# Kernel optimization log

Hardware: AMD Instinct MI355X
Metric: run time of the kernel (lower is better)

Reference implementation:

```python
import jax, jax.numpy as jnp
import numpy as np

DIM = 4096
N_HEADS = 32
N_KV = 8
HD = 128
SW = 4096          # sliding window / cache length
B = 32             # max_batch_size (decode batch)
MAX_SEQ = 8192
START_POS = 4000
CURRENT_POS = 4000

def _nearest_32(n):
    return ((n + 31) // 32) * 32

PADDED_LEN = min(_nearest_32(START_POS + 1), SW)  # 4032

def _rope_tables():
    inv_freq = 1.0 / (10000.0 ** (np.arange(0, HD, 2, dtype=np.float32) / HD))
    t = np.arange(MAX_SEQ, dtype=np.float32)
    freqs = np.outer(t, inv_freq)                       # [MAX_SEQ, HD/2]
    emb = np.concatenate([freqs, freqs], axis=-1)       # [MAX_SEQ, HD]
    return jnp.asarray(np.cos(emb)), jnp.asarray(np.sin(emb))

def rotate_half(u):
    u1, u2 = jnp.split(u, 2, axis=-1)
    return jnp.concatenate([-u2, u1], axis=-1)

def setup_inputs() -> dict:
    key = jax.random.key(0)
    ks = jax.random.split(key, 6)
    cos_cached, sin_cached = _rope_tables()
    return {
        "x": jax.random.normal(ks[0], (1, 1, B, DIM), jnp.float32),
        "wqkv": jax.random.normal(ks[1], (DIM, DIM + 2 * N_KV * HD), jnp.float32) * 0.02,
        "wo": jax.random.normal(ks[2], (DIM, DIM), jnp.float32) * 0.02,
        "cache_k": jax.random.normal(ks[3], (B, N_KV, SW, HD), jnp.float32) * 0.5,
        "cache_v": jax.random.normal(ks[4], (B, N_KV, SW, HD), jnp.float32) * 0.5,
        "cos_cached": cos_cached,
        "sin_cached": sin_cached,
        "attn_mask": jnp.zeros((B, N_HEADS, 1, PADDED_LEN), jnp.float32),
        "start_pos": START_POS,
        "current_pos": CURRENT_POS,
    }

def reference(x, wqkv, wo, cache_k, cache_v, cos_cached, sin_cached, attn_mask,
              start_pos, current_pos):
    group = N_HEADS // N_KV
    padded_len = min(_nearest_32(start_pos + 1), SW)
    scale = 1.0 / jnp.sqrt(jnp.float32(HD))

    # fused QKV projection: x (1,1,B,DIM) @ wqkv -> (B, DIM + 2*N_KV*HD)
    xqkv = x[0, 0] @ wqkv
    q = xqkv[:, :DIM].reshape(B, N_HEADS, HD)
    k = xqkv[:, DIM:DIM + N_KV * HD].reshape(B, N_KV, HD)
    v = xqkv[:, DIM + N_KV * HD:].reshape(B, N_KV, HD)

    # rotary embedding at position start_pos (single decode token)
    cos = cos_cached[start_pos]   # [HD]
    sin = sin_cached[start_pos]
    q = q * cos + rotate_half(q) * sin
    k = k * cos + rotate_half(k) * sin

    # sliding-window KV cache update at current_pos
    cache_k = cache_k.at[:, :, current_pos, :].set(k)
    cache_v = cache_v.at[:, :, current_pos, :].set(v)
    keys = cache_k[:, :, :padded_len, :]     # [B, N_KV, L, HD]
    values = cache_v[:, :, :padded_len, :]

    # grouped attention: q heads grouped by kv head
    qg = q.reshape(B, N_KV, group, HD)
    scores = jnp.einsum('bkgd,bkld->bkgl', qg, keys) * scale
    scores = scores + attn_mask.reshape(B, N_KV, group, padded_len)
    probs = jax.nn.softmax(scores, axis=-1)
    out = jnp.einsum('bkgl,bkld->bkgd', probs, values)   # [B, N_KV, group, HD]

    # concat heads and output projection
    dense = out.reshape(B, DIM) @ wo
    return dense.reshape(1, 1, B, DIM)
```

## Files before the change

kernel.cpp:

```cpp
#include <hip/hip_runtime.h>
#include <hip/hip_bf16.h>

typedef unsigned int u32;
typedef unsigned short u16;

__device__ __forceinline__ u16 f2bf(float f){ u32 x; __builtin_memcpy(&x,&f,4); u32 r=(x+0x7fffu+((x>>16)&1u))>>16; return (u16)r; }
__device__ __forceinline__ float lo2f(u32 u){ u32 x=u<<16; float f; __builtin_memcpy(&f,&x,4); return f; }
__device__ __forceinline__ float hi2f(u32 u){ u32 x=u&0xffff0000u; float f; __builtin_memcpy(&f,&x,4); return f; }

__global__ __launch_bounds__(256) void transpose_x(
    const float* __restrict__ x, float* __restrict__ xt)
{
    __shared__ float ld[32][65];
    const int t = threadIdx.x;
    const int g = blockIdx.x;
    #pragma unroll
    for (int i=0;i<8;++i) {
        const int e = i*256 + t;
        const int b = e >> 6, dd = e & 63;
        ld[b][dd] = x[(size_t)b*4096 + g*64 + dd];
    }
    __syncthreads();
    #pragma unroll
    for (int i=0;i<8;++i) {
        const int e = i*256 + t;
        const int dd = e >> 5, b = e & 31;
        xt[(size_t)(g*64 + dd)*32 + b] = ld[b][dd];
    }
}

__global__ __launch_bounds__(256) void gemm_splitk_t(
    const float* __restrict__ At, const float2* __restrict__ W2,
    float* __restrict__ P, int K, int N, int dps)
{
    const int j2 = blockIdx.x*256 + threadIdx.x;
    const int s = blockIdx.y;
    float acc0[32], acc1[32];
    #pragma unroll
    for (int b=0;b<32;++b){ acc0[b]=0.f; acc1[b]=0.f; }
    const int d0 = s*dps, d1 = d0 + dps;
    const int halfN = N >> 1;
    #pragma unroll 2
    for (int d=d0; d<d1; ++d) {
        const float2 wv = W2[(size_t)d*halfN + j2];
        const float* __restrict__ Ad = At + d*32;
        #pragma unroll
        for (int b=0;b<32;++b) {
            const float av = Ad[b];
            acc0[b] = fmaf(av, wv.x, acc0[b]);
            acc1[b] = fmaf(av, wv.y, acc1[b]);
        }
    }
    float* Pp = P + (size_t)(s*32)*N + 2*j2;
    #pragma unroll
    for (int b=0;b<32;++b)
        *reinterpret_cast<float2*>(Pp + (size_t)b*N) = make_float2(acc0[b], acc1[b]);
}

__global__ __launch_bounds__(256) void qkv_finish(
    const float* __restrict__ P, const float* __restrict__ cosc,
    const float* __restrict__ sinc, const int* __restrict__ spp,
    float* __restrict__ qws, float* __restrict__ kn, float* __restrict__ vn,
    int splits)
{
    __shared__ float sh[256];
    const int t = threadIdx.x;
    const int col = blockIdx.x*256 + t;
    const int b = blockIdx.y;
    float v = 0.f;
    for (int s=0;s<splits;++s) v += P[(size_t)(s*32+b)*6144 + col];
    sh[t] = v;
    __syncthreads();
    if (col < 5120) {
        const int d = col & 127;
        const int pt = (t & ~127) | ((d<64)? d+64 : d-64);
        const float pv = sh[pt];
        const int spos = *spp;
        const float c  = cosc[spos*128 + d];
        const float sn = sinc[spos*128 + d];
        const float rot = (d<64)? -pv : pv;
        const float val = fmaf(v, c, rot*sn);
        if (col < 4096) qws[(size_t)b*4096 + col] = val;
        else            kn[(size_t)b*1024 + (col-4096)] = val;
    } else {
        vn[(size_t)b*1024 + (col-5120)] = v;
    }
}

__global__ __launch_bounds__(1024, 4) void attn_kernel(
    const float* __restrict__ qws, const float* __restrict__ Kc,
    const float* __restrict__ Vc, const float* __restrict__ kn,
    const float* __restrict__ vn, const float* __restrict__ mask,
    const int* __restrict__ curp, float* __restrict__ aout_t,
    const int PL, const int SW)
{
    __shared__ uint2 probsP[4096];
    __shared__ float obuf[16][4][128];
    __shared__ float redm[16][4];
    __shared__ float reds[16][4];

    const int t = threadIdx.x;
    const int lane = t & 63;
    const int w = t >> 6;
    const int b  = blockIdx.x >> 3;
    const int kv = blockIdx.x & 7;
    const int cur = *curp;

    const size_t mat = (size_t)(b*8+kv);
    const float* __restrict__ Kb  = Kc + mat*(size_t)SW*128;
    const float* __restrict__ knr = kn + mat*128;
    const float* __restrict__ qbase = qws + (size_t)(b*32 + kv*4)*128;

    float s[4][4];
    #pragma unroll
    for (int i=0;i<4;++i) {
        const int p = i*1024 + t;
        float acc0=0.f, acc1=0.f, acc2=0.f, acc3=0.f;
        if (p < PL) {
            const float* __restrict__ row = (p==cur) ? knr : (Kb + (size_t)p*128);
            #pragma unroll
            for (int dc=0; dc<16; ++dc) {
                const float4 ka = *reinterpret_cast<const float4*>(row + dc*8);
                const float4 kb = *reinterpret_cast<const float4*>(row + dc*8 + 4);
                const float* __restrict__ q0 = qbase + dc*8;
                #pragma unroll
                for (int j=0;j<4;++j) {
                    const float kj = (j==0)?ka.x:(j==1)?ka.y:(j==2)?ka.z:ka.w;
                    acc0 = fmaf(q0[j      ], kj, acc0);
                    acc1 = fmaf(q0[j+128  ], kj, acc1);
                    acc2 = fmaf(q0[j+256  ], kj, acc2);
                    acc3 = fmaf(q0[j+384  ], kj, acc3);
                }
                #pragma unroll
                for (int j=0;j<4;++j) {
                    const float kj = (j==0)?kb.x:(j==1)?kb.y:(j==2)?kb.z:kb.w;
                    acc0 = fmaf(q0[j+4    ], kj, acc0);
                    acc1 = fmaf(q0[j+132  ], kj, acc1);
                    acc2 = fmaf(q0[j+260  ], kj, acc2);
                    acc3 = fmaf(q0[j+388  ], kj, acc3);
                }
            }
        }
        s[0][i]=acc0; s[1][i]=acc1; s[2][i]=acc2; s[3][i]=acc3;
    }

    const float scale = 0.08838834764831845f;
    const size_t mbase = ((size_t)b*32 + (size_t)kv*4)*(size_t)PL;
    #pragma unroll
    for (int i=0;i<4;++i) {
        const int p = i*1024 + t;
        if (p < PL) {
            #pragma unroll
            for (int h=0;h<4;++h) {
                const float mv = mask[mbase + (size_t)h*PL + p];
                s[h][i] = fmaf(s[h][i], scale, mv);
            }
        } else {
            #pragma unroll
            for (int h=0;h<4;++h) s[h][i] = -3.0e38f;
        }
    }

    float lm[4];
    #pragma unroll
    for (int h=0;h<4;++h) {
        lm[h] = fmaxf(fmaxf(s[h][0],s[h][1]), fmaxf(s[h][2],s[h][3]));
    }
    #pragma unroll
    for (int off=1; off<64; off<<=1) {
        #pragma unroll
        for (int h=0;h<4;++h) lm[h] = fmaxf(lm[h], __shfl_xor(lm[h], off, 64));
    }
    if (lane==0) {
        #pragma unroll
        for (int h=0;h<4;++h) redm[w][h] = lm[h];
    }
    __syncthreads();
    float M[4];
    #pragma unroll
    for (int h=0;h<4;++h) {
        float m = redm[0][h];
        #pragma unroll
        for (int ww=1;ww<16;++ww) m = fmaxf(m, redm[ww][h]);
        M[h] = m;
    }

    float ls[4] = {0.f,0.f,0.f,0.f};
    #pragma unroll
    for (int i=0;i<4;++i) {
        #pragma unroll
        for (int h=0;h<4;++h) {
            const float e = __expf(s[h][i] - M[h]);
            s[h][i] = e;
            ls[h] += e;
        }
    }
    #pragma unroll
    for (int off=1; off<64; off<<=1) {
        #pragma unroll
        for (int h=0;h<4;++h) ls[h] += __shfl_xor(ls[h], off, 64);
    }
    if (lane==0) {
        #pragma unroll
        for (int h=0;h<4;++h) reds[w][h] = ls[h];
    }
    __syncthreads();
    float inv[4];
    #pragma unroll
    for (int h=0;h<4;++h) {
        float sm = reds[0][h];
        #pragma unroll
        for (int ww=1;ww<16;++ww) sm += reds[ww][h];
        inv[h] = 1.f / sm;
    }

    #pragma unroll
    for (int i=0;i<4;++i) {
        const int p = i*1024 + t;
        if (p < PL) {
            const u32 plo = (u32)f2bf(s[0][i]*inv[0]) | ((u32)f2bf(s[1][i]*inv[1]) << 16);
            const u32 phi = (u32)f2bf(s[2][i]*inv[2]) | ((u32)f2bf(s[3][i]*inv[3]) << 16);
            probsP[p] = make_uint2(plo, phi);
        }
    }
    __syncthreads();

    const float* __restrict__ Vb  = Vc + mat*(size_t)SW*128;
    const float* __restrict__ vnr = vn + mat*128;
    const int chunk = PL >> 4;
    const int p0 = w*chunk, p1 = p0 + chunk;
    float a0[4] = {0.f,0.f,0.f,0.f}, a1[4] = {0.f,0.f,0.f,0.f};
    #pragma unroll 8
    for (int p=p0; p<p1; ++p) {
        const float* row = (p==cur) ? vnr : (Vb + (size_t)p*128);
        const float2 vv = *reinterpret_cast<const float2*>(row + 2*lane);
        const uint2 pp = probsP[p];
        const float pr0 = lo2f(pp.x), pr1 = hi2f(pp.x);
        const float pr2 = lo2f(pp.y), pr3 = hi2f(pp.y);
        a0[0]=fmaf(pr0,vv.x,a0[0]); a1[0]=fmaf(pr0,vv.y,a1[0]);
        a0[1]=fmaf(pr1,vv.x,a0[1]); a1[1]=fmaf(pr1,vv.y,a1[1]);
        a0[2]=fmaf(pr2,vv.x,a0[2]); a1[2]=fmaf(pr2,vv.y,a1[2]);
        a0[3]=fmaf(pr3,vv.x,a0[3]); a1[3]=fmaf(pr3,vv.y,a1[3]);
    }
    #pragma unroll
    for (int h=0;h<4;++h)
        *reinterpret_cast<float2*>(&obuf[w][h][2*lane]) = make_float2(a0[h], a1[h]);
    __syncthreads();

    if (t < 512) {
        const int h = t >> 7;
        const int d = t & 127;
        float sum = obuf[0][h][d];
        #pragma unroll
        for (int ww=1;ww<16;++ww) sum += obuf[ww][h][d];
        const int col = (kv*4 + h)*128 + d;
        aout_t[(size_t)col*32 + b] = sum;
    }
}

__global__ __launch_bounds__(256) void wo_finish(
    const float* __restrict__ P, float* __restrict__ out, int splits)
{
    const int col = blockIdx.x*256 + threadIdx.x;
    const int b = blockIdx.y;
    float v = 0.f;
    for (int s=0;s<splits;++s) v += P[(size_t)(s*32+b)*4096 + col];
    out[(size_t)b*4096 + col] = v;
}

extern "C" void kernel_launch(void* const* d_in, const int* in_sizes, int n_in,
                              void* d_out, int out_size, void* d_ws, size_t ws_size,
                              hipStream_t stream)
{
    const float* x    = (const float*)d_in[0];
    const float* wqkv = (const float*)d_in[1];
    const float* wo   = (const float*)d_in[2];
    const float* cK   = (const float*)d_in[3];
    const float* cV   = (const float*)d_in[4];
    const float* cosc = (const float*)d_in[5];
    const float* sinc = (const float*)d_in[6];
    const float* mask = (const float*)d_in[7];
    const int* sp   = (const int*)d_in[8];
    const int* cp   = (const int*)d_in[9];

    const int PL = in_sizes[7] / (32*32);
    const int SW = in_sizes[3] / (32*8*128);

    char* ws = (char*)d_ws;
    float* xt    = (float*)(ws);
    float* qws   = (float*)(ws + 524288);
    float* aout_t= (float*)(ws + 2*524288);
    float* kn    = (float*)(ws + 3*524288);
    float* vn    = (float*)(ws + 3*524288 + 131072);
    float* Pbuf  = (float*)(ws + 3*524288 + 2*131072);

    int splits = 64;
    {
        const size_t fixed = 3ull*524288 + 2ull*131072;
        while (splits > 4 && fixed + (size_t)splits*32*6144*4 > ws_size) splits >>= 1;
    }
    const int dps = 4096 / splits;

    transpose_x<<<64, 256, 0, stream>>>(x, xt);
    gemm_splitk_t<<<dim3(12, splits), 256, 0, stream>>>(xt, (const float2*)wqkv, Pbuf, 4096, 6144, dps);
    qkv_finish<<<dim3(24, 32), 256, 0, stream>>>(Pbuf, cosc, sinc, sp, qws, kn, vn, splits);

    attn_kernel<<<256, 1024, 0, stream>>>(qws, cK, cV, kn, vn, mask, cp, aout_t, PL, SW);

    gemm_splitk_t<<<dim3(8, splits), 256, 0, stream>>>(aout_t, (const float2*)wo, Pbuf, 4096, 4096, dps);
    wo_finish<<<dim3(16, 32), 256, 0, stream>>>(Pbuf, (float*)d_out, splits);
}
```

Before: 338.7 us.

## Compute QK scores with 16-lane cooperative coalesced K row reads into LDS

```diff
diff --git a/kernel.cpp b/kernel.cpp
--- a/kernel.cpp
+++ b/kernel.cpp
@@ -94,6 +94,7 @@
     const int* __restrict__ curp, float* __restrict__ aout_t,
     const int PL, const int SW)
 {
+    __shared__ float scoresS[4*4100];
     __shared__ uint2 probsP[4096];
     __shared__ float obuf[16][4][128];
     __shared__ float redm[16][4];
@@ -111,41 +112,50 @@
     const float* __restrict__ knr = kn + mat*128;
     const float* __restrict__ qbase = qws + (size_t)(b*32 + kv*4)*128;
 
-    float s[4][4];
-    #pragma unroll
-    for (int i=0;i<4;++i) {
-        const int p = i*1024 + t;
-        float acc0=0.f, acc1=0.f, acc2=0.f, acc3=0.f;
-        if (p < PL) {
-            const float* __restrict__ row = (p==cur) ? knr : (Kb + (size_t)p*128);
-            #pragma unroll
-            for (int dc=0; dc<16; ++dc) {
-                const float4 ka = *reinterpret_cast<const float4*>(row + dc*8);
-                const float4 kb = *reinterpret_cast<const float4*>(row + dc*8 + 4);
-                const float* __restrict__ q0 = qbase + dc*8;
-                #pragma unroll
-                for (int j=0;j<4;++j) {
-                    const float kj = (j==0)?ka.x:(j==1)?ka.y:(j==2)?ka.z:ka.w;
-                    acc0 = fmaf(q0[j      ], kj, acc0);
-                    acc1 = fmaf(q0[j+128  ], kj, acc1);
-                    acc2 = fmaf(q0[j+256  ], kj, acc2);
-                    acc3 = fmaf(q0[j+384  ], kj, acc3);
-                }
-                #pragma unroll
-                for (int j=0;j<4;++j) {
-                    const float kj = (j==0)?kb.x:(j==1)?kb.y:(j==2)?kb.z:kb.w;
-                    acc0 = fmaf(q0[j+4    ], kj, acc0);
-                    acc1 = fmaf(q0[j+132  ], kj, acc1);
-                    acc2 = fmaf(q0[j+260  ], kj, acc2);
-                    acc3 = fmaf(q0[j+388  ], kj, acc3);
-                }
-            }
-        }
-        s[0][i]=acc0; s[1][i]=acc1; s[2][i]=acc2; s[3][i]=acc3;
-    }
+    const int l   = lane & 15;
+    const int grp = lane >> 4;
+    float qv[4][8];
+    #pragma unroll
+    for (int h=0;h<4;++h)
+        #pragma unroll
+        for (int j=0;j<8;++j)
+            qv[h][j] = qbase[h*128 + l*8 + j];
+
+    const int rpw = PL >> 4;
+    const int rb0 = w * rpw;
+    for (int g=0; g<rpw; g+=4) {
+        const int r = rb0 + g + grp;
+        const float* __restrict__ row = (r==cur) ? knr : (Kb + (size_t)r*128);
+        const float4 ka = *reinterpret_cast<const float4*>(row + l*8);
+        const float4 kb4 = *reinterpret_cast<const float4*>(row + l*8 + 4);
+        float kf[8];
+        kf[0]=ka.x; kf[1]=ka.y; kf[2]=ka.z; kf[3]=ka.w;
+        kf[4]=kb4.x; kf[5]=kb4.y; kf[6]=kb4.z; kf[7]=kb4.w;
+        float sc0=0.f, sc1=0.f, sc2=0.f, sc3=0.f;
+        #pragma unroll
+        for (int j=0;j<8;++j) {
+            sc0 = fmaf(qv[0][j], kf[j], sc0);
+            sc1 = fmaf(qv[1][j], kf[j], sc1);
+            sc2 = fmaf(qv[2][j], kf[j], sc2);
+            sc3 = fmaf(qv[3][j], kf[j], sc3);
+        }
+        #pragma unroll
+        for (int off=8; off; off>>=1) {
+            sc0 += __shfl_xor(sc0, off, 16);
+            sc1 += __shfl_xor(sc1, off, 16);
+            sc2 += __shfl_xor(sc2, off, 16);
+            sc3 += __shfl_xor(sc3, off, 16);
+        }
+        if (l < 4) {
+            const float v = (l==0)?sc0:(l==1)?sc1:(l==2)?sc2:sc3;
+            scoresS[l*4100 + r] = v;
+        }
+    }
+    __syncthreads();
 
     const float scale = 0.08838834764831845f;
     const size_t mbase = ((size_t)b*32 + (size_t)kv*4)*(size_t)PL;
+    float s[4][4];
     #pragma unroll
     for (int i=0;i<4;++i) {
         const int p = i*1024 + t;
@@ -153,7 +163,7 @@
             #pragma unroll
             for (int h=0;h<4;++h) {
                 const float mv = mask[mbase + (size_t)h*PL + p];
-                s[h][i] = fmaf(s[h][i], scale, mv);
+                s[h][i] = fmaf(scoresS[h*4100 + p], scale, mv);
             }
         } else {
             #pragma unroll
@@ -163,9 +173,8 @@
 
     float lm[4];
     #pragma unroll
-    for (int h=0;h<4;++h) {
+    for (int h=0;h<4;++h)
         lm[h] = fmaxf(fmaxf(s[h][0],s[h][1]), fmaxf(s[h][2],s[h][3]));
-    }
     #pragma unroll
     for (int off=1; off<64; off<<=1) {
         #pragma unroll
```

Result: faster. 305.0 us (-10.0%).
